# Kernel optimization log

Hardware: AMD Instinct MI355X
Metric: run time of the kernel (lower is better)

The kernel has to match this reference:

```python
import jax, jax.numpy as jnp
import numpy as np

N_VERTS = 778
N_JOINTS_CHAIN = 16  # wrist + 15 articulated joints
N_JOINTS_ALL = 21
PARENTS = np.array([0, 0, 1, 2, 0, 4, 5, 0, 7, 8, 0, 10, 11, 0, 13, 14])


def rodrigues(r):
    """Axis-angle [N,3] -> rotation matrices [N,3,3] (matches torch quat2mat path)."""
    angle = jnp.linalg.norm(r + 1e-8, axis=1, keepdims=True)  # [N,1]
    axis = r / angle
    c = jnp.cos(angle)[..., None]  # [N,1,1]
    s = jnp.sin(angle)[..., None]
    x, y, z = axis[:, 0], axis[:, 1], axis[:, 2]
    zero = jnp.zeros_like(x)
    K = jnp.stack([zero, -z, y,
                   z, zero, -x,
                   -y, x, zero], axis=1).reshape(-1, 3, 3)
    eye = jnp.eye(3, dtype=r.dtype)
    return eye + s * K + (1.0 - c) * jnp.matmul(K, K)


def make_A(R, t):
    """R [B,3,3], t [B,3] -> homogeneous [B,4,4]."""
    B = R.shape[0]
    top = jnp.concatenate([R, t[:, :, None]], axis=2)  # [B,3,4]
    bottom = jnp.broadcast_to(jnp.array([[[0., 0., 0., 1.]]], dtype=R.dtype), (B, 1, 4))
    return jnp.concatenate([top, bottom], axis=1)


def setup_inputs() -> dict:
    key = jax.random.key(0)
    ks = jax.random.split(key, 10)
    B = 8192
    w = jax.random.uniform(ks[9], (N_VERTS, 16), dtype=jnp.float32)
    w = w / jnp.sum(w, axis=1, keepdims=True)  # LBS weights rows sum to 1
    Jr = jax.random.uniform(ks[6], (N_VERTS, N_JOINTS_ALL), dtype=jnp.float32)
    Jr = Jr / jnp.sum(Jr, axis=0, keepdims=True)
    return {
        "beta": jax.random.normal(ks[0], (B, 10), dtype=jnp.float32) * 0.5,
        "theta": jax.random.normal(ks[1], (B, 10), dtype=jnp.float32) * 0.5,
        "wrist_euler": jax.random.normal(ks[2], (B, 3), dtype=jnp.float32) * 0.3,
        "v_template": jax.random.normal(ks[3], (N_VERTS, 3), dtype=jnp.float32) * 0.05,
        "shapedirs": jax.random.normal(ks[4], (10, N_VERTS * 3), dtype=jnp.float32) * 0.01,
        "posedirs": jax.random.normal(ks[5], (135, N_VERTS * 3), dtype=jnp.float32) * 0.01,
        "J_regressor": Jr,
        "hands_comp": jax.random.normal(ks[7], (10, 45), dtype=jnp.float32) * 0.5,
        "hands_mean": jax.random.normal(ks[8], (45,), dtype=jnp.float32) * 0.1,
        "weights": w,
    }


def reference(beta, theta, wrist_euler, v_template, shapedirs, posedirs,
              J_regressor, hands_comp, hands_mean, weights):
    B = beta.shape[0]
    # shape blendshapes
    v_shaped = jnp.matmul(beta, shapedirs).reshape(B, N_VERTS, 3) + v_template
    # joints from shaped template: [B,21,3]
    J = jnp.einsum('bvc,vj->bjc', v_shaped, J_regressor)
    # pca pose -> per-joint axis-angle -> rotation matrices
    euler_pose = jnp.matmul(theta, hands_comp) + hands_mean          # [B,45]
    Rs = rodrigues(euler_pose.reshape(-1, 3)).reshape(B, 15, 3, 3)
    global_rot = rodrigues(wrist_euler.reshape(-1, 3)).reshape(B, 1, 3, 3)
    # pose blendshapes: (Rs - I) flattened
    pose_feature = (Rs - jnp.eye(3, dtype=Rs.dtype)).reshape(B, 135)
    v_posed = v_shaped + jnp.matmul(pose_feature, posedirs).reshape(B, N_VERTS, 3)
    # kinematic chain (16 joints, fixed small loop)
    Rs_all = jnp.concatenate([global_rot, Rs], axis=1)  # [B,16,3,3]
    Jc = J[:, :N_JOINTS_CHAIN, :]
    results = [make_A(Rs_all[:, 0], Jc[:, 0])]
    for i in range(1, N_JOINTS_CHAIN):
        p = int(PARENTS[i])
        A_local = make_A(Rs_all[:, i], Jc[:, i] - Jc[:, p])
        results.append(jnp.matmul(results[p], A_local))
    G = jnp.stack(results, axis=1)  # [B,16,4,4]
    # subtract rest-pose joint locations: A = G - G @ [J;0] in last column
    Jh = jnp.concatenate([Jc, jnp.zeros((B, N_JOINTS_CHAIN, 1), Jc.dtype)], axis=2)
    GJ = jnp.einsum('bjpq,bjq->bjp', G, Jh)  # [B,16,4]
    A = G - jnp.concatenate([jnp.zeros((B, N_JOINTS_CHAIN, 4, 3), G.dtype), GJ[..., None]], axis=3)
    # linear blend skinning
    T = jnp.einsum('vj,bjpq->bvpq', weights, A)  # [B,778,4,4]
    v_posed_h = jnp.concatenate([v_posed, jnp.ones((B, N_VERTS, 1), v_posed.dtype)], axis=2)
    verts = jnp.einsum('bvpq,bvq->bvp', T, v_posed_h)[:, :, :3]
    joints = jnp.einsum('bvc,vj->bjc', verts, J_regressor)  # [B,21,3]
    return joints
```

## Files before the change

### kernel.cpp

```cpp
#include <hip/hip_runtime.h>
#include <math.h>

#define NV 778
#define KROW 2334
#define KTOT 146
#define KLD  148
#define NCOL 1008
#define NPART 32
#define DTLD 160
#define PEXLD 1032

__global__ __launch_bounds__(64) void kA_pre(const float* __restrict__ shapedirs,
                                             const float* __restrict__ posedirs,
                                             const float* __restrict__ v_template,
                                             const float* __restrict__ Jreg,
                                             const float* __restrict__ wgt,
                                             float* __restrict__ SJ, float* __restrict__ J0,
                                             float* __restrict__ Q,  float* __restrict__ W2,
                                             float* __restrict__ DT, int w2_blocks)
{
    const int bid = blockIdx.x;
    const int t = threadIdx.x;
    if (bid < 48) {
        const int j = bid / 3, c = bid % 3;
        float acc[11];
#pragma unroll
        for (int k = 0; k < 11; ++k) acc[k] = 0.f;
        for (int v = t; v < NV; v += 64) {
            const float jr = Jreg[v*21 + j];
            acc[10] += v_template[v*3 + c] * jr;
#pragma unroll
            for (int k = 0; k < 10; ++k)
                acc[k] += shapedirs[(size_t)k*KROW + v*3 + c] * jr;
        }
#pragma unroll
        for (int k = 0; k < 11; ++k) {
            float s = acc[k];
#pragma unroll
            for (int off = 32; off >= 1; off >>= 1) s += __shfl_down(s, off, 64);
            acc[k] = s;
        }
        if (t == 0) {
#pragma unroll
            for (int k = 0; k < 10; ++k) SJ[k*48 + j*3 + c] = acc[k];
            J0[j*3 + c] = acc[10];
        }
    } else if (bid < 384) {
        const int m = bid - 48, j = m >> 4, jj = m & 15;
        float s = 0.f;
        for (int v = t; v < NV; v += 64)
            s += Jreg[v*21 + j] * wgt[v*16 + jj];
#pragma unroll
        for (int off = 32; off >= 1; off >>= 1) s += __shfl_down(s, off, 64);
        if (t == 0) Q[m] = s;
    } else if (bid < 384 + w2_blocks) {
        const int gi = (bid - 384)*64 + t;
        if (gi < NV*336) {
            const int v = gi / 336, m = gi % 336;
            const int j = m >> 4, jj = m & 15;
            W2[gi] = Jreg[v*21 + j] * wgt[v*16 + jj];
        }
    } else {
        const int v = bid - 384 - w2_blocks;
#pragma unroll
        for (int kk = 0; kk < 3; ++kk) {
            const int k = t + kk*64;
            if (k < KTOT) {
                const float* drow = (k < 10)  ? shapedirs + (size_t)k*KROW
                                  : (k < 145) ? posedirs + (size_t)(k-10)*KROW
                                              : v_template;
                DT[((size_t)0*NV + v)*DTLD + k] = drow[3*v + 0];
                DT[((size_t)1*NV + v)*DTLD + k] = drow[3*v + 1];
                DT[((size_t)2*NV + v)*DTLD + k] = drow[3*v + 2];
            }
        }
    }
}

__global__ __launch_bounds__(256) void k_mid(const float* __restrict__ DT,
                                             const float* __restrict__ W2,
                                             float* __restrict__ PKpartT,
                                             const float* __restrict__ beta,
                                             const float* __restrict__ theta,
                                             const float* __restrict__ wrist,
                                             const float* __restrict__ hc,
                                             const float* __restrict__ hm,
                                             const float* __restrict__ SJ,
                                             const float* __restrict__ J0,
                                             float* __restrict__ coefT,
                                             float* __restrict__ A_g, int B)
{
    __shared__ float Rs[16*144];
    __shared__ float cls[16*148];
    const int bid = blockIdx.x;
    const int t = threadIdx.x;

    if (bid < 21*3*NPART) {
        const int j = bid % 21;
        const int c = (bid / 21) % 3;
        const int s = bid / 63;
        const int k = t;
        if (k >= KTOT) return;
        float acc[16];
#pragma unroll
        for (int q = 0; q < 16; ++q) acc[q] = 0.f;
        const int v0 = s*25, v1 = min(NV, v0 + 25);
        const float* dt = DT + ((size_t)c*NV)*DTLD + k;
        for (int v = v0; v < v1; ++v) {
            const float d = dt[(size_t)v*DTLD];
            const float4* wq = (const float4*)(W2 + (size_t)v*336 + j*16);
            const float4 w0 = wq[0], w1 = wq[1], w2 = wq[2], w3 = wq[3];
            acc[0]  += d*w0.x; acc[1]  += d*w0.y; acc[2]  += d*w0.z; acc[3]  += d*w0.w;
            acc[4]  += d*w1.x; acc[5]  += d*w1.y; acc[6]  += d*w1.z; acc[7]  += d*w1.w;
            acc[8]  += d*w2.x; acc[9]  += d*w2.y; acc[10] += d*w2.z; acc[11] += d*w2.w;
            acc[12] += d*w3.x; acc[13] += d*w3.y; acc[14] += d*w3.z; acc[15] += d*w3.w;
        }
        float* o = PKpartT + ((size_t)s*NCOL + j*48 + c)*KLD + k;
#pragma unroll
        for (int q = 0; q < 16; ++q) o[(size_t)q*3*KLD] = acc[q];
        return;
    }

    const int kb = bid - 21*3*NPART;
    const int bl = t >> 4, i = t & 15;
    const int b = kb*16 + bl;

    float r0, r1, r2;
    if (i == 0) {
        r0 = wrist[b*3+0]; r1 = wrist[b*3+1]; r2 = wrist[b*3+2];
#pragma unroll
        for (int k = 0; k < 10; ++k) cls[bl*148 + k] = beta[b*10 + k];
        cls[bl*148 + 145] = 1.0f;
    } else {
        const int col = (i-1)*3;
        float e0 = hm[col], e1 = hm[col+1], e2 = hm[col+2];
#pragma unroll
        for (int k = 0; k < 10; ++k) {
            const float th = theta[b*10 + k];
            e0 += th * hc[k*45 + col];
            e1 += th * hc[k*45 + col+1];
            e2 += th * hc[k*45 + col+2];
        }
        r0 = e0; r1 = e1; r2 = e2;
    }
    const float x_ = r0 + 1e-8f, y_ = r1 + 1e-8f, z_ = r2 + 1e-8f;
    const float angle = sqrtf(x_*x_ + y_*y_ + z_*z_);
    const float inv = 1.0f / angle;
    const float x = r0*inv, y = r1*inv, z = r2*inv;
    const float sn = sinf(angle), cs = cosf(angle);
    const float t1 = 1.0f - cs;
    float R[9];
    R[0] = 1.f - t1*(y*y + z*z);
    R[1] = -sn*z + t1*x*y;
    R[2] =  sn*y + t1*x*z;
    R[3] =  sn*z + t1*x*y;
    R[4] = 1.f - t1*(x*x + z*z);
    R[5] = -sn*x + t1*y*z;
    R[6] = -sn*y + t1*x*z;
    R[7] =  sn*x + t1*y*z;
    R[8] = 1.f - t1*(x*x + y*y);
#pragma unroll
    for (int q = 0; q < 9; ++q) Rs[bl*144 + i*9 + q] = R[q];
    if (i > 0) {
#pragma unroll
        for (int q = 0; q < 9; ++q)
            cls[bl*148 + 10 + (i-1)*9 + q] = R[q] - ((q==0||q==4||q==8) ? 1.f : 0.f);
    }
    __syncthreads();

    if (t < KTOT) {
        float tmp[16];
#pragma unroll
        for (int m = 0; m < 16; ++m) tmp[m] = cls[m*148 + t];
        float4* dst = (float4*)(coefT + (size_t)t*B + kb*16);
        dst[0] = make_float4(tmp[0],  tmp[1],  tmp[2],  tmp[3]);
        dst[1] = make_float4(tmp[4],  tmp[5],  tmp[6],  tmp[7]);
        dst[2] = make_float4(tmp[8],  tmp[9],  tmp[10], tmp[11]);
        dst[3] = make_float4(tmp[12], tmp[13], tmp[14], tmp[15]);
    }

    if (t < 16) {
        const int b2 = kb*16 + t;
        float bt[10];
#pragma unroll
        for (int k = 0; k < 10; ++k) bt[k] = beta[b2*10 + k];
        const float* Rb = Rs + t*144;
        float4* Ab = (float4*)(A_g + (size_t)b2*192);

        auto jointJ = [&](int j, float* o) {
            float j0 = J0[j*3+0], j1 = J0[j*3+1], j2 = J0[j*3+2];
#pragma unroll
            for (int k = 0; k < 10; ++k) {
                j0 += bt[k] * SJ[k*48 + j*3 + 0];
                j1 += bt[k] * SJ[k*48 + j*3 + 1];
                j2 += bt[k] * SJ[k*48 + j*3 + 2];
            }
            o[0] = j0; o[1] = j1; o[2] = j2;
        };

        float G0R[9], J0v[3];
#pragma unroll
        for (int q = 0; q < 9; ++q) G0R[q] = Rb[q];
        jointJ(0, J0v);
#pragma unroll
        for (int r = 0; r < 3; ++r) {
            const float at = J0v[r] - (G0R[r*3+0]*J0v[0] + G0R[r*3+1]*J0v[1] + G0R[r*3+2]*J0v[2]);
            Ab[r] = make_float4(G0R[r*3+0], G0R[r*3+1], G0R[r*3+2], at);
        }
        for (int ch = 0; ch < 5; ++ch) {
            float GpR[9], Gpt[3], Jp[3];
#pragma unroll
            for (int q = 0; q < 9; ++q) GpR[q] = G0R[q];
            Gpt[0]=J0v[0]; Gpt[1]=J0v[1]; Gpt[2]=J0v[2];
            Jp[0]=J0v[0];  Jp[1]=J0v[1];  Jp[2]=J0v[2];
            for (int s = 0; s < 3; ++s) {
                const int j = ch*3 + 1 + s;
                float Rl[9];
                const float* Rj = Rb + j*9;
#pragma unroll
                for (int q = 0; q < 9; ++q) Rl[q] = Rj[q];
                float Jc[3];
                jointJ(j, Jc);
                const float tl0 = Jc[0]-Jp[0], tl1 = Jc[1]-Jp[1], tl2 = Jc[2]-Jp[2];
                float GR[9], Gt[3];
#pragma unroll
                for (int r = 0; r < 3; ++r) {
#pragma unroll
                    for (int cc = 0; cc < 3; ++cc)
                        GR[r*3+cc] = GpR[r*3+0]*Rl[0*3+cc] + GpR[r*3+1]*Rl[1*3+cc] + GpR[r*3+2]*Rl[2*3+cc];
                    Gt[r] = GpR[r*3+0]*tl0 + GpR[r*3+1]*tl1 + GpR[r*3+2]*tl2 + Gpt[r];
                }
#pragma unroll
                for (int r = 0; r < 3; ++r) {
                    const float at = Gt[r] - (GR[r*3+0]*Jc[0] + GR[r*3+1]*Jc[1] + GR[r*3+2]*Jc[2]);
                    Ab[j*3 + r] = make_float4(GR[r*3+0], GR[r*3+1], GR[r*3+2], at);
                }
#pragma unroll
                for (int q = 0; q < 9; ++q) GpR[q] = GR[q];
                Gpt[0]=Gt[0]; Gpt[1]=Gt[1]; Gpt[2]=Gt[2];
                Jp[0]=Jc[0];  Jp[1]=Jc[1];  Jp[2]=Jc[2];
            }
        }
    }
}

__global__ __launch_bounds__(256) void k_p3(const float4* __restrict__ PKpartT4,
                                            float* __restrict__ PK)
{
    const int n4s = NCOL*(KLD/4);
    const int idx = blockIdx.x*256 + threadIdx.x;
    if (idx >= n4s) return;
    const int col = idx / (KLD/4);
    const int k4  = idx % (KLD/4);
    float4 s = PKpartT4[idx];
#pragma unroll
    for (int p = 1; p < NPART; ++p) {
        const float4 v = PKpartT4[(size_t)p*n4s + idx];
        s.x += v.x; s.y += v.y; s.z += v.z; s.w += v.w;
    }
    const int k = k4*4;
    const float sv[4] = {s.x, s.y, s.z, s.w};
#pragma unroll
    for (int e = 0; e < 4; ++e)
        if (k + e < KTOT) PK[(size_t)(k + e)*NCOL + col] = sv[e];
}

__global__ __launch_bounds__(512) void k3_gemm(const float* __restrict__ coefT,
                                               const float* __restrict__ PK,
                                               const float* __restrict__ A_g,
                                               const float* __restrict__ Q,
                                               float* __restrict__ out, int B)
{
    __shared__ float Pex[8*PEXLD];
    const int t  = threadIdx.x;
    const int b0 = blockIdx.x * 16;
    const int l  = t;

    float acc[2][16];
#pragma unroll
    for (int e = 0; e < 16; ++e) { acc[0][e] = 0.f; acc[1][e] = 0.f; }

    if (l < 504) {
        const float* pkp = PK + 2*l;
        const float* cof = coefT + b0;
#pragma unroll 2
        for (int k = 0; k < KTOT; ++k) {
            const float2 p2 = *(const float2*)(pkp + (size_t)k*NCOL);
            const float4* cp = (const float4*)(cof + (size_t)k*B);
            const float4 c0 = cp[0], c1 = cp[1], c2 = cp[2], c3 = cp[3];
            const float cv[16] = {c0.x,c0.y,c0.z,c0.w, c1.x,c1.y,c1.z,c1.w,
                                  c2.x,c2.y,c2.z,c2.w, c3.x,c3.y,c3.z,c3.w};
#pragma unroll
            for (int e = 0; e < 16; ++e) {
                acc[0][e] += p2.x * cv[e];
                acc[1][e] += p2.y * cv[e];
            }
        }
    }

#pragma unroll
    for (int r = 0; r < 2; ++r) {
        __syncthreads();
        if (l < 504) {
            const int j  = (2*l) / 48;
            const int sc = j*49 + (2*l - 48*j);
#pragma unroll
            for (int bb = 0; bb < 8; ++bb)
                *(float2*)(&Pex[bb*PEXLD + sc]) =
                    make_float2(acc[0][r*8 + bb], acc[1][r*8 + bb]);
        }
        __syncthreads();
        if (t < 504) {
            const int bl = t / 63;
            const int rm = t % 63;
            const int j  = rm / 3, p = rm % 3;
            const int b  = b0 + r*8 + bl;
            const float4* Ab = ((const float4*)A_g) + (size_t)b*48;
            const float* Pr = Pex + bl*PEXLD + j*49;
            float s = 0.f;
#pragma unroll
            for (int jj = 0; jj < 16; ++jj) {
                const float4 a = Ab[jj*3 + p];
                s += a.x*Pr[jj*3+0] + a.y*Pr[jj*3+1] + a.z*Pr[jj*3+2]
                   + a.w*Q[j*16+jj];
            }
            out[(size_t)b0*63 + r*504 + t] = s;
        }
    }
}

extern "C" void kernel_launch(void* const* d_in, const int* in_sizes, int n_in,
                              void* d_out, int out_size, void* d_ws, size_t ws_size,
                              hipStream_t stream) {
    (void)n_in; (void)out_size; (void)ws_size;
    const float* beta       = (const float*)d_in[0];
    const float* theta      = (const float*)d_in[1];
    const float* wrist      = (const float*)d_in[2];
    const float* v_template = (const float*)d_in[3];
    const float* shapedirs  = (const float*)d_in[4];
    const float* posedirs   = (const float*)d_in[5];
    const float* Jreg       = (const float*)d_in[6];
    const float* hc         = (const float*)d_in[7];
    const float* hm         = (const float*)d_in[8];
    const float* wgt        = (const float*)d_in[9];
    float* out = (float*)d_out;
    const int B = in_sizes[0] / 10;

    float* ws = (float*)d_ws;
    size_t off = 0;
    auto alloc = [&](size_t n) { float* p = ws + off; off = (off + n + 63) & ~(size_t)63; return p; };
    float* SJ      = alloc(480);
    float* J0      = alloc(48);
    float* Q       = alloc(336);
    float* W2      = alloc((size_t)NV*336);
    float* DT      = alloc((size_t)3*NV*DTLD);
    float* PKpartT = alloc((size_t)NPART*NCOL*KLD);
    float* PK      = alloc((size_t)KTOT*NCOL);
    float* coefT   = alloc((size_t)KTOT*B);
    float* A_g     = alloc((size_t)B*192);

    const int w2_blocks = (NV*336 + 63)/64;
    const int nb_mid = 21*3*NPART + (B + 15)/16;
    const int nb_p3  = (NCOL*(KLD/4) + 255)/256;

    kA_pre<<<384 + w2_blocks + NV, 64, 0, stream>>>(shapedirs, posedirs, v_template,
                                                    Jreg, wgt, SJ, J0, Q, W2, DT, w2_blocks);
    k_mid<<<nb_mid, 256, 0, stream>>>(DT, W2, PKpartT, beta, theta, wrist, hc, hm,
                                      SJ, J0, coefT, A_g, B);
    k_p3<<<nb_p3, 256, 0, stream>>>((const float4*)PKpartT, PK);
    k3_gemm<<<dim3(B/16), 512, 0, stream>>>(coefT, PK, A_g, Q, out, B);
}
```

Before: 149.8 us.

## Run main GEMM on bf16 MFMA with split-bf16 hi/lo operand emulation

Replaces the scalar FP32 FMA GEMM in k3_gemm with 16x16x32 bf16 MFMA instructions. Each FP32 operand is split into a bf16 hi and lo part, and the K dimension is laid out as three segments (hi*hi, lo*hi, hi*lo) so the accumulation approximates FP32 precision. coefA and PK are stored as row-major bf16 arrays padded to 448, and all 16 batch rows are staged in shared memory in one pass. It trades a 3x larger K and some accuracy loss from the dropped lo*lo term for matrix-core throughput.

```diff
diff --git a/kernel.cpp b/kernel.cpp
--- a/kernel.cpp
+++ b/kernel.cpp
@@ -5,10 +5,23 @@
 #define KROW 2334
 #define KTOT 146
 #define KLD  148
+#define KSPL 448
 #define NCOL 1008
 #define NPART 32
 #define DTLD 160
-#define PEXLD 1032
+#define PEXLD2 1034
+
+typedef __attribute__((ext_vector_type(8))) short short8v;
+typedef __attribute__((ext_vector_type(4))) float f32x4;
+
+__device__ __forceinline__ unsigned short f2bf(float x) {
+    unsigned int u = __float_as_uint(x);
+    u += 0x7FFF + ((u >> 16) & 1);
+    return (unsigned short)(u >> 16);
+}
+__device__ __forceinline__ float bf2f(unsigned short h) {
+    return __uint_as_float((unsigned int)h << 16);
+}
 
 __global__ __launch_bounds__(64) void kA_pre(const float* __restrict__ shapedirs,
                                              const float* __restrict__ posedirs,
@@ -87,7 +100,7 @@
                                              const float* __restrict__ hm,
                                              const float* __restrict__ SJ,
                                              const float* __restrict__ J0,
-                                             float* __restrict__ coefT,
+                                             unsigned short* __restrict__ coefA,
                                              float* __restrict__ A_g, int B)
 {
     __shared__ float Rs[16*144];
@@ -168,15 +181,17 @@
     }
     __syncthreads();
 
-    if (t < KTOT) {
-        float tmp[16];
-#pragma unroll
-        for (int m = 0; m < 16; ++m) tmp[m] = cls[m*148 + t];
-        float4* dst = (float4*)(coefT + (size_t)t*B + kb*16);
-        dst[0] = make_float4(tmp[0],  tmp[1],  tmp[2],  tmp[3]);
-        dst[1] = make_float4(tmp[4],  tmp[5],  tmp[6],  tmp[7]);
-        dst[2] = make_float4(tmp[8],  tmp[9],  tmp[10], tmp[11]);
-        dst[3] = make_float4(tmp[12], tmp[13], tmp[14], tmp[15]);
+    {
+        unsigned short* ca = coefA + (size_t)b*KSPL;
+        for (int k = i; k < KTOT; k += 16) {
+            const float xv = cls[bl*148 + k];
+            const unsigned short hi = f2bf(xv);
+            const unsigned short lo = f2bf(xv - bf2f(hi));
+            ca[k]       = hi;
+            ca[146 + k] = lo;
+            ca[292 + k] = hi;
+        }
+        if (i < 10) ca[438 + i] = 0;
     }
 
     if (t < 16) {
@@ -245,7 +260,7 @@
 }
 
 __global__ __launch_bounds__(256) void k_p3(const float4* __restrict__ PKpartT4,
-                                            float* __restrict__ PK)
+                                            unsigned short* __restrict__ PKb)
 {
     const int n4s = NCOL*(KLD/4);
     const int idx = blockIdx.x*256 + threadIdx.x;
@@ -258,71 +273,81 @@
         const float4 v = PKpartT4[(size_t)p*n4s + idx];
         s.x += v.x; s.y += v.y; s.z += v.z; s.w += v.w;
     }
+    unsigned short* pb = PKb + (size_t)col*KSPL;
     const int k = k4*4;
     const float sv[4] = {s.x, s.y, s.z, s.w};
 #pragma unroll
-    for (int e = 0; e < 4; ++e)
-        if (k + e < KTOT) PK[(size_t)(k + e)*NCOL + col] = sv[e];
-}
-
-__global__ __launch_bounds__(512) void k3_gemm(const float* __restrict__ coefT,
-                                               const float* __restrict__ PK,
+    for (int e = 0; e < 4; ++e) {
+        if (k + e < KTOT) {
+            const unsigned short hi = f2bf(sv[e]);
+            const unsigned short lo = f2bf(sv[e] - bf2f(hi));
+            pb[k+e]       = hi;
+            pb[146 + k+e] = hi;
+            pb[292 + k+e] = lo;
+        }
+    }
+    if (k4 == 0) {
+#pragma unroll
+        for (int z = 0; z < 10; ++z) pb[438 + z] = 0;
+    }
+}
+
+__global__ __launch_bounds__(512) void k3_gemm(const unsigned short* __restrict__ coefA,
+                                               const unsigned short* __restrict__ PKb,
                                                const float* __restrict__ A_g,
                                                const float* __restrict__ Q,
                                                float* __restrict__ out, int B)
 {
-    __shared__ float Pex[8*PEXLD];
+    __shared__ float Pex[16*PEXLD2];
     const int t  = threadIdx.x;
     const int b0 = blockIdx.x * 16;
-    const int l  = t;
-
-    float acc[2][16];
-#pragma unroll
-    for (int e = 0; e < 16; ++e) { acc[0][e] = 0.f; acc[1][e] = 0.f; }
-
-    if (l < 504) {
-        const float* pkp = PK + 2*l;
-        const float* cof = coefT + b0;
-#pragma unroll 2
-        for (int k = 0; k < KTOT; ++k) {
-            const float2 p2 = *(const float2*)(pkp + (size_t)k*NCOL);
-            const float4* cp = (const float4*)(cof + (size_t)k*B);
-            const float4 c0 = cp[0], c1 = cp[1], c2 = cp[2], c3 = cp[3];
-            const float cv[16] = {c0.x,c0.y,c0.z,c0.w, c1.x,c1.y,c1.z,c1.w,
-                                  c2.x,c2.y,c2.z,c2.w, c3.x,c3.y,c3.z,c3.w};
-#pragma unroll
-            for (int e = 0; e < 16; ++e) {
-                acc[0][e] += p2.x * cv[e];
-                acc[1][e] += p2.y * cv[e];
-            }
-        }
-    }
+    const int w  = t >> 6, l = t & 63;
+    const int lr = l & 15, lk = (l >> 4) * 8;
+
+    short8v a[14];
+    {
+        const unsigned short* ar = coefA + (size_t)(b0 + lr)*KSPL + lk;
+#pragma unroll
+        for (int s = 0; s < 14; ++s) a[s] = *(const short8v*)(ar + s*32);
+    }
+
+#pragma unroll
+    for (int u = 0; u < 8; ++u) {
+        const int tt = w*8 + u;
+        if (tt < 63) {
+            f32x4 acc = {0.f, 0.f, 0.f, 0.f};
+            const unsigned short* br = PKb + (size_t)(tt*16 + lr)*KSPL + lk;
+#pragma unroll
+            for (int s = 0; s < 14; ++s) {
+                const short8v bf = *(const short8v*)(br + s*32);
+                acc = __builtin_amdgcn_mfma_f32_16x16x32_bf16(a[s], bf, acc, 0, 0, 0);
+            }
+            const int ct = tt*16 + lr;
+            const int j  = ct / 48;
+            const int sc = j*49 + (ct - 48*j);
+            const int rb = (l >> 4) * 4;
+#pragma unroll
+            for (int r = 0; r < 4; ++r)
+                Pex[(rb + r)*PEXLD2 + sc] = acc[r];
+        }
+    }
+    __syncthreads();
 
 #pragma unroll
     for (int r = 0; r < 2; ++r) {
-        __syncthreads();
-        if (l < 504) {
-            const int j  = (2*l) / 48;
-            const int sc = j*49 + (2*l - 48*j);
-#pragma unroll
-            for (int bb = 0; bb < 8; ++bb)
-                *(float2*)(&Pex[bb*PEXLD + sc]) =
-                    make_float2(acc[0][r*8 + bb], acc[1][r*8 + bb]);
-        }
-        __syncthreads();
         if (t < 504) {
             const int bl = t / 63;
             const int rm = t % 63;
             const int j  = rm / 3, p = rm % 3;
             const int b  = b0 + r*8 + bl;
             const float4* Ab = ((const float4*)A_g) + (size_t)b*48;
-            const float* Pr = Pex + bl*PEXLD + j*49;
+            const float* Pr = Pex + (r*8 + bl)*PEXLD2 + j*49;
             float s = 0.f;
 #pragma unroll
             for (int jj = 0; jj < 16; ++jj) {
-                const float4 a = Ab[jj*3 + p];
-                s += a.x*Pr[jj*3+0] + a.y*Pr[jj*3+1] + a.z*Pr[jj*3+2]
-                   + a.w*Q[j*16+jj];
+                const float4 aa = Ab[jj*3 + p];
+                s += aa.x*Pr[jj*3+0] + aa.y*Pr[jj*3+1] + aa.z*Pr[jj*3+2]
+                   + aa.w*Q[j*16+jj];
             }
             out[(size_t)b0*63 + r*504 + t] = s;
         }
@@ -355,8 +380,8 @@
     float* W2      = alloc((size_t)NV*336);
     float* DT      = alloc((size_t)3*NV*DTLD);
     float* PKpartT = alloc((size_t)NPART*NCOL*KLD);
-    float* PK      = alloc((size_t)KTOT*NCOL);
-    float* coefT   = alloc((size_t)KTOT*B);
+    unsigned short* PKb   = (unsigned short*)alloc((size_t)NCOL*KSPL/2);
+    unsigned short* coefA = (unsigned short*)alloc((size_t)B*KSPL/2);
     float* A_g     = alloc((size_t)B*192);
 
     const int w2_blocks = (NV*336 + 63)/64;
@@ -366,7 +391,7 @@
     kA_pre<<<384 + w2_blocks + NV, 64, 0, stream>>>(shapedirs, posedirs, v_template,
                                                     Jreg, wgt, SJ, J0, Q, W2, DT, w2_blocks);
     k_mid<<<nb_mid, 256, 0, stream>>>(DT, W2, PKpartT, beta, theta, wrist, hc, hm,
-                                      SJ, J0, coefT, A_g, B);
-    k_p3<<<nb_p3, 256, 0, stream>>>((const float4*)PKpartT, PK);
-    k3_gemm<<<dim3(B/16), 512, 0, stream>>>(coefT, PK, A_g, Q, out, B);
-}
+                                      SJ, J0, coefA, A_g, B);
+    k_p3<<<nb_p3, 256, 0, stream>>>((const float4*)PKpartT, PKb);
+    k3_gemm<<<dim3(B/16), 512, 0, stream>>>(coefA, PKb, A_g, Q, out, B);
+}
```

New measurement: 177.2 us. 18.3% more time.

## Stage PK rows through double-buffered shared memory in k3_gemm

Applied to the files above, without the earlier changes.

The GEMM kernel now loads PK in chunks of 4 k-rows into a double-buffered LDS tile, prefetching the next chunk into registers while computing the current one, instead of each thread reading PK directly from global memory. K is padded to 148 with zeroed rows in both coefT and PK so chunks divide evenly. The k_p3 reduction kernel now uses 64-thread blocks. This trades extra shared memory and barriers per chunk for fewer redundant global loads of PK across blocks.

```diff
diff --git a/kernel.cpp b/kernel.cpp
--- a/kernel.cpp
+++ b/kernel.cpp
@@ -9,6 +9,8 @@
 #define NPART 32
 #define DTLD 160
 #define PEXLD 1032
+#define CK   4
+#define NCHUNK (KLD/CK)
 
 __global__ __launch_bounds__(64) void kA_pre(const float* __restrict__ shapedirs,
                                              const float* __restrict__ posedirs,
@@ -178,6 +180,9 @@
         dst[2] = make_float4(tmp[8],  tmp[9],  tmp[10], tmp[11]);
         dst[3] = make_float4(tmp[12], tmp[13], tmp[14], tmp[15]);
     }
+    if (t < 32) {
+        coefT[(size_t)(KTOT + (t >> 4))*B + kb*16 + (t & 15)] = 0.f;
+    }
 
     if (t < 16) {
         const int b2 = kb*16 + t;
@@ -244,11 +249,11 @@
     }
 }
 
-__global__ __launch_bounds__(256) void k_p3(const float4* __restrict__ PKpartT4,
-                                            float* __restrict__ PK)
+__global__ __launch_bounds__(64) void k_p3(const float4* __restrict__ PKpartT4,
+                                           float* __restrict__ PK)
 {
     const int n4s = NCOL*(KLD/4);
-    const int idx = blockIdx.x*256 + threadIdx.x;
+    const int idx = blockIdx.x*64 + threadIdx.x;
     if (idx >= n4s) return;
     const int col = idx / (KLD/4);
     const int k4  = idx % (KLD/4);
@@ -262,40 +267,68 @@
     const float sv[4] = {s.x, s.y, s.z, s.w};
 #pragma unroll
     for (int e = 0; e < 4; ++e)
-        if (k + e < KTOT) PK[(size_t)(k + e)*NCOL + col] = sv[e];
+        PK[(size_t)(k + e)*NCOL + col] = (k + e < KTOT) ? sv[e] : 0.f;
 }
 
-__global__ __launch_bounds__(512) void k3_gemm(const float* __restrict__ coefT,
-                                               const float* __restrict__ PK,
-                                               const float* __restrict__ A_g,
-                                               const float* __restrict__ Q,
-                                               float* __restrict__ out, int B)
+__global__ __launch_bounds__(512, 4) void k3_gemm(const float* __restrict__ coefT,
+                                                  const float* __restrict__ PK,
+                                                  const float* __restrict__ A_g,
+                                                  const float* __restrict__ Q,
+                                                  float* __restrict__ out, int B)
 {
+    __shared__ float buf[2][CK*1024];
     __shared__ float Pex[8*PEXLD];
     const int t  = threadIdx.x;
     const int b0 = blockIdx.x * 16;
     const int l  = t;
+    const float* cof = coefT + b0;
 
     float acc[2][16];
 #pragma unroll
     for (int e = 0; e < 16; ++e) { acc[0][e] = 0.f; acc[1][e] = 0.f; }
 
-    if (l < 504) {
-        const float* pkp = PK + 2*l;
-        const float* cof = coefT + b0;
-#pragma unroll 2
-        for (int k = 0; k < KTOT; ++k) {
-            const float2 p2 = *(const float2*)(pkp + (size_t)k*NCOL);
-            const float4* cp = (const float4*)(cof + (size_t)k*B);
+    {
+        const float4* s4 = (const float4*)PK;
+        const float4 v0 = s4[t], v1 = s4[t + 512];
+        *(float4*)&buf[0][4*t] = v0;
+        *(float4*)&buf[0][4*t + 2048] = v1;
+    }
+    __syncthreads();
+
+    for (int c = 0; c < NCHUNK; ++c) {
+        float4 n0, n1;
+        const bool have = (c + 1 < NCHUNK);
+        if (have) {
+            const float4* s4 = (const float4*)(PK + (size_t)(c+1)*CK*NCOL);
+            n0 = s4[t]; n1 = s4[t + 512];
+        }
+        float cv[CK][16];
+#pragma unroll
+        for (int kk = 0; kk < CK; ++kk) {
+            const float4* cp = (const float4*)(cof + (size_t)(c*CK + kk)*B);
             const float4 c0 = cp[0], c1 = cp[1], c2 = cp[2], c3 = cp[3];
-            const float cv[16] = {c0.x,c0.y,c0.z,c0.w, c1.x,c1.y,c1.z,c1.w,
-                                  c2.x,c2.y,c2.z,c2.w, c3.x,c3.y,c3.z,c3.w};
-#pragma unroll
-            for (int e = 0; e < 16; ++e) {
-                acc[0][e] += p2.x * cv[e];
-                acc[1][e] += p2.y * cv[e];
+            cv[kk][0]=c0.x;  cv[kk][1]=c0.y;  cv[kk][2]=c0.z;  cv[kk][3]=c0.w;
+            cv[kk][4]=c1.x;  cv[kk][5]=c1.y;  cv[kk][6]=c1.z;  cv[kk][7]=c1.w;
+            cv[kk][8]=c2.x;  cv[kk][9]=c2.y;  cv[kk][10]=c2.z; cv[kk][11]=c2.w;
+            cv[kk][12]=c3.x; cv[kk][13]=c3.y; cv[kk][14]=c3.z; cv[kk][15]=c3.w;
+        }
+        if (l < 504) {
+#pragma unroll
+            for (int kk = 0; kk < CK; ++kk) {
+                const float2 p2 = *(const float2*)&buf[c & 1][kk*NCOL + 2*l];
+#pragma unroll
+                for (int e = 0; e < 16; ++e) {
+                    acc[0][e] += p2.x * cv[kk][e];
+                    acc[1][e] += p2.y * cv[kk][e];
+                }
             }
         }
+        __syncthreads();
+        if (have) {
+            *(float4*)&buf[(c+1) & 1][4*t] = n0;
+            *(float4*)&buf[(c+1) & 1][4*t + 2048] = n1;
+        }
+        __syncthreads();
     }
 
 #pragma unroll
@@ -355,18 +388,18 @@
     float* W2      = alloc((size_t)NV*336);
     float* DT      = alloc((size_t)3*NV*DTLD);
     float* PKpartT = alloc((size_t)NPART*NCOL*KLD);
-    float* PK      = alloc((size_t)KTOT*NCOL);
-    float* coefT   = alloc((size_t)KTOT*B);
+    float* PK      = alloc((size_t)KLD*NCOL + 128);
+    float* coefT   = alloc((size_t)KLD*B);
     float* A_g     = alloc((size_t)B*192);
 
     const int w2_blocks = (NV*336 + 63)/64;
     const int nb_mid = 21*3*NPART + (B + 15)/16;
-    const int nb_p3  = (NCOL*(KLD/4) + 255)/256;
+    const int nb_p3  = (NCOL*(KLD/4) + 63)/64;
 
     kA_pre<<<384 + w2_blocks + NV, 64, 0, stream>>>(shapedirs, posedirs, v_template,
                                                     Jreg, wgt, SJ, J0, Q, W2, DT, w2_blocks);
     k_mid<<<nb_mid, 256, 0, stream>>>(DT, W2, PKpartT, beta, theta, wrist, hc, hm,
                                       SJ, J0, coefT, A_g, B);
-    k_p3<<<nb_p3, 256, 0, stream>>>((const float4*)PKpartT, PK);
+    k_p3<<<nb_p3, 64, 0, stream>>>((const float4*)PKpartT, PK);
     k3_gemm<<<dim3(B/16), 512, 0, stream>>>(coefT, PK, A_g, Q, out, B);
 }
```

Result: slower. 159.3 us (+6.4%).
